# Kernel optimization log

Measured on AMD Instinct MI355X. Metric: run time of the kernel, lower is better.

## Reference

```python
import jax, jax.numpy as jnp
import numpy as np

N_HEADS = 8
D_K = 64
SCALE = D_K ** -0.5


def setup_inputs() -> dict:
    key = jax.random.key(0)
    ks = jax.random.split(key, 5)
    B, C, H, W = 4, 512, 32, 32
    x = jax.random.normal(ks[0], (B, C, H, W), dtype=jnp.float32)
    Wp = jax.random.normal(ks[1], (3 * N_HEADS * D_K, C), dtype=jnp.float32) * (C ** -0.5)
    bp = jax.random.normal(ks[2], (3 * N_HEADS * D_K,), dtype=jnp.float32) * 0.02
    Wo = jax.random.normal(ks[3], (C, N_HEADS * D_K), dtype=jnp.float32) * ((N_HEADS * D_K) ** -0.5)
    bo = jax.random.normal(ks[4], (C,), dtype=jnp.float32) * 0.02
    return {"x": x, "Wp": Wp, "bp": bp, "Wo": Wo, "bo": bo}


def reference(x, Wp, bp, Wo, bo):
    # x: [B, C, H, W]; NOTE: the torch module defines GroupNorm but never calls it.
    B, C, H, W = x.shape
    s = H * W
    xs = x.reshape(B, C, s).transpose(0, 2, 1)          # [B, s, C]
    qkv = (xs @ Wp.T + bp).reshape(B, s, N_HEADS, 3 * D_K)
    q, k, v = jnp.split(qkv, 3, axis=-1)                 # each [B, s, h, d]
    attn = jnp.einsum('bihd,bjhd->bijh', q, k) * SCALE   # [B, s, s, h]
    attn = jax.nn.softmax(attn, axis=2)                  # softmax over j (keys)
    res = jnp.einsum('bijh,bjhd->bihd', attn, v)         # [B, s, h, d]
    res = res.reshape(B, s, N_HEADS * D_K)
    out = res @ Wo.T + bo + xs                           # residual add
    return out.transpose(0, 2, 1).reshape(B, C, H, W)
```

## Files before the change

### kernel.cpp

```cpp
#include <hip/hip_runtime.h>
#include <hip/hip_bf16.h>

typedef unsigned short u16;
typedef __attribute__((ext_vector_type(8))) short frag_ab;
typedef __attribute__((ext_vector_type(4))) float f32x4;
typedef _Float16 f16;
typedef __attribute__((ext_vector_type(4))) _Float16 f16x4;

#define LOG2E 1.44269504088896f

__device__ __forceinline__ float fast_exp2(float x) {
    return __builtin_amdgcn_exp2f(x);
}

__device__ __forceinline__ void gload_lds16(const u16* g, u16* s) {
    __builtin_amdgcn_global_load_lds((const __attribute__((address_space(1))) void*)g,
                                     (__attribute__((address_space(3))) void*)s, 16, 0, 0);
}
__device__ __forceinline__ void gload_lds16h(const f16* g, f16* s) {
    __builtin_amdgcn_global_load_lds((const __attribute__((address_space(1))) void*)g,
                                     (__attribute__((address_space(3))) void*)s, 16, 0, 0);
}

__device__ __forceinline__ void gemm64x128_bt_mainloop(
    const u16* __restrict__ A, const u16* __restrict__ B, int K,
    int m0, int n0, f32x4 acc[2][4], u16* As, u16* Bs)
{
    const int tid = threadIdx.x;
    const int lane = tid & 63, quad = lane >> 4, l16 = lane & 15;
    const int wr = ((tid >> 7) & 1) * 32;
    const int wc = ((tid >> 6) & 1) * 64;
    const int srow = tid >> 3;
    const int scol = (tid & 7) * 8;

    for (int k0 = 0; k0 < K; k0 += 64) {
        __syncthreads();
        #pragma unroll
        for (int p = 0; p < 2; ++p) {
            const int r = srow + p * 32;
            gload_lds16(A + (size_t)(m0 + r) * K + k0 + scol, As + r * 64 + scol);
        }
        #pragma unroll
        for (int p = 0; p < 4; ++p) {
            const int r = srow + p * 32;
            gload_lds16(B + (size_t)(n0 + r) * K + k0 + scol, Bs + r * 64 + scol);
        }
        __syncthreads();
        #pragma unroll
        for (int ks = 0; ks < 2; ++ks) {
            frag_ab a[2], b[4];
            #pragma unroll
            for (int mt = 0; mt < 2; ++mt)
                a[mt] = *(const frag_ab*)(As + (wr + mt * 16 + l16) * 64 + ks * 32 + quad * 8);
            #pragma unroll
            for (int nt = 0; nt < 4; ++nt)
                b[nt] = *(const frag_ab*)(Bs + (wc + nt * 16 + l16) * 64 + ks * 32 + quad * 8);
            #pragma unroll
            for (int mt = 0; mt < 2; ++mt)
                #pragma unroll
                for (int nt = 0; nt < 4; ++nt)
                    acc[mt][nt] = __builtin_amdgcn_mfma_f32_16x16x32_bf16(a[mt], b[nt], acc[mt][nt], 0, 0, 0);
        }
    }
}

__device__ __forceinline__ void gemm64x64_bt_mainloop(
    const u16* __restrict__ A, const u16* __restrict__ B, int K,
    int m0, int n0, f32x4 acc[2][2], u16* As, u16* Bs)
{
    const int tid = threadIdx.x;
    const int lane = tid & 63, quad = lane >> 4, l16 = lane & 15;
    const int wr = ((tid >> 7) & 1) * 32;
    const int wc = ((tid >> 6) & 1) * 32;
    const int srow = tid >> 3;
    const int scol = (tid & 7) * 8;

    for (int k0 = 0; k0 < K; k0 += 64) {
        __syncthreads();
        #pragma unroll
        for (int p = 0; p < 2; ++p) {
            const int r = srow + p * 32;
            gload_lds16(A + (size_t)(m0 + r) * K + k0 + scol, As + r * 64 + scol);
            gload_lds16(B + (size_t)(n0 + r) * K + k0 + scol, Bs + r * 64 + scol);
        }
        __syncthreads();
        #pragma unroll
        for (int ks = 0; ks < 2; ++ks) {
            frag_ab a[2], b[2];
            #pragma unroll
            for (int mt = 0; mt < 2; ++mt)
                a[mt] = *(const frag_ab*)(As + (wr + mt * 16 + l16) * 64 + ks * 32 + quad * 8);
            #pragma unroll
            for (int nt = 0; nt < 2; ++nt)
                b[nt] = *(const frag_ab*)(Bs + (wc + nt * 16 + l16) * 64 + ks * 32 + quad * 8);
            #pragma unroll
            for (int mt = 0; mt < 2; ++mt)
                #pragma unroll
                for (int nt = 0; nt < 2; ++nt)
                    acc[mt][nt] = __builtin_amdgcn_mfma_f32_16x16x32_bf16(a[mt], b[nt], acc[mt][nt], 0, 0, 0);
        }
    }
}

__global__ __launch_bounds__(256) void prep_kernel(
    const float* __restrict__ x, __hip_bfloat16* __restrict__ xs_bf,
    const float* __restrict__ Wp, const float* __restrict__ Wo,
    __hip_bfloat16* __restrict__ w_bf)
{
    __shared__ float tile[32][33];
    const int tid = threadIdx.x;
    const int id = blockIdx.x;
    if (id < 2048) {
        const int i0 = (id & 31) * 32;
        const int c0 = ((id >> 5) & 15) * 32;
        const int b  = id >> 9;
        const int tx = tid & 31, ty = tid >> 5;
        const float* xp = x + ((size_t)b * 512 + c0) * 1024 + i0;
        #pragma unroll
        for (int r = ty; r < 32; r += 8)
            tile[r][tx] = xp[(size_t)r * 1024 + tx];
        __syncthreads();
        __hip_bfloat16* op = xs_bf + ((size_t)b * 1024 + i0) * 512 + c0;
        #pragma unroll
        for (int r = ty; r < 32; r += 8)
            op[(size_t)r * 512 + tx] = __float2bfloat16(tile[tx][r]);
    } else {
        const int t = (id - 2048) * 256 + tid;
        const int i4 = t * 4;
        const float* src = (i4 < 786432) ? (Wp + i4) : (Wo + (i4 - 786432));
        const float4 v = *(const float4*)src;
        ushort4 o;
        o.x = __bfloat16_as_ushort(__float2bfloat16(v.x));
        o.y = __bfloat16_as_ushort(__float2bfloat16(v.y));
        o.z = __bfloat16_as_ushort(__float2bfloat16(v.z));
        o.w = __bfloat16_as_ushort(__float2bfloat16(v.w));
        *(ushort4*)((u16*)w_bf + i4) = o;
    }
}

__global__ __launch_bounds__(256) void qkv_gemm_kernel(
    const u16* __restrict__ Wpb, const u16* __restrict__ xsb,
    const float* __restrict__ bp,
    u16* __restrict__ Qb, u16* __restrict__ Kb, f16* __restrict__ VtT)
{
    __shared__ u16 lds[12288];
    u16* As = lds;
    u16* Bs = lds + 4096;
    f32x4 acc[2][4];
    #pragma unroll
    for (int mt = 0; mt < 2; ++mt)
        #pragma unroll
        for (int nt = 0; nt < 4; ++nt)
            { acc[mt][nt][0]=0.f; acc[mt][nt][1]=0.f; acc[mt][nt][2]=0.f; acc[mt][nt][3]=0.f; }
    const int m0 = blockIdx.x * 64;
    const int n0 = blockIdx.y * 128;
    gemm64x128_bt_mainloop(Wpb, xsb, 512, m0, n0, acc, As, Bs);

    const int tid = threadIdx.x;
    const int lane = tid & 63, quad = lane >> 4, l16 = lane & 15;
    const int wr = ((tid >> 7) & 1) * 32, wc = ((tid >> 6) & 1) * 64;
    const int h = blockIdx.x / 3, part = blockIdx.x % 3;
    const int b = blockIdx.y >> 3, ipb = (blockIdx.y & 7) * 128;
    const size_t bh = (size_t)(b * 8 + h);

    if (part < 2) {
        const float scale = (part == 0) ? (0.125f * LOG2E) : 1.0f;
        __syncthreads();
        u16* T = lds;
        #pragma unroll
        for (int nt = 0; nt < 4; ++nt) {
            const int px = wc + nt * 16 + l16;
            #pragma unroll
            for (int mt = 0; mt < 2; ++mt) {
                const int cb = m0 + wr + mt * 16 + quad * 4;
                ushort4 pk;
                pk.x = __bfloat16_as_ushort(__float2bfloat16((acc[mt][nt][0] + bp[cb + 0]) * scale));
                pk.y = __bfloat16_as_ushort(__float2bfloat16((acc[mt][nt][1] + bp[cb + 1]) * scale));
                pk.z = __bfloat16_as_ushort(__float2bfloat16((acc[mt][nt][2] + bp[cb + 2]) * scale));
                pk.w = __bfloat16_as_ushort(__float2bfloat16((acc[mt][nt][3] + bp[cb + 3]) * scale));
                *(ushort4*)&T[px * 72 + wr + mt * 16 + quad * 4] = pk;
            }
        }
        __syncthreads();
        u16* dst = (part == 0 ? Qb : Kb);
        #pragma unroll
        for (int p = 0; p < 4; ++p) {
            const int row = p * 32 + (tid >> 3);
            const int ch8 = (tid & 7) * 8;
            uint4 rv = *(uint4*)&T[row * 72 + ch8];
            *(uint4*)(dst + ((bh * 1024 + ipb + row) << 6) + ch8) = rv;
        }
    } else {
        f16* dst = VtT + bh * 65536;
        #pragma unroll
        for (int mt = 0; mt < 2; ++mt) {
            #pragma unroll
            for (int r = 0; r < 4; ++r) {
                const int d = wr + mt * 16 + quad * 4 + r;
                const float bias = bp[m0 + d];
                #pragma unroll
                for (int nt = 0; nt < 4; ++nt) {
                    const int j = ipb + wc + nt * 16 + l16;
                    dst[(size_t)(j >> 3) * 512 + d * 8 + (j & 7)] =
                        (f16)(acc[mt][nt][r] + bias);
                }
            }
        }
    }
}

__global__ __launch_bounds__(256) void attn_kernel(
    const u16* __restrict__ Qb, const u16* __restrict__ Kb,
    const f16* __restrict__ VtT, __hip_bfloat16* __restrict__ resb)
{
    __shared__ u16 Ks[128 * 64];
    __shared__ f16 Vs[16 * 64 * 8];
    __shared__ float Opart[4][32][68];
    __shared__ float Lpart[4][4][16];
    const int bh = blockIdx.x;
    const int it = blockIdx.y;
    const int tid = threadIdx.x;
    const int w = tid >> 6, lane = tid & 63, quad = lane >> 4, l16 = lane & 15;
    const int srow = tid >> 3, scol = (tid & 7) * 8;

    const u16* Qp = Qb + (size_t)bh * 65536;
    const u16* Kp = Kb + (size_t)bh * 65536;
    const f16* Vp = VtT + (size_t)bh * 65536;

    frag_ab bq[4][2];
    #pragma unroll
    for (int ig = 0; ig < 4; ++ig) {
        const u16* qptr = Qp + (size_t)(it * 64 + ig * 16 + l16) * 64 + quad * 8;
        bq[ig][0] = *(const frag_ab*)(qptr);
        bq[ig][1] = *(const frag_ab*)(qptr + 32);
    }

    f32x4 o[4][4];
    #pragma unroll
    for (int ig = 0; ig < 4; ++ig)
        #pragma unroll
        for (int dt = 0; dt < 4; ++dt)
            { o[ig][dt][0]=0.f; o[ig][dt][1]=0.f; o[ig][dt][2]=0.f; o[ig][dt][3]=0.f; }
    float l_acc[4] = {0.f, 0.f, 0.f, 0.f};

    for (int jt = 0; jt < 8; ++jt) {
        __syncthreads();
        #pragma unroll
        for (int p = 0; p < 4; ++p) {
            const int r = srow + p * 32;
            gload_lds16(Kp + (size_t)(jt * 128 + r) * 64 + scol, Ks + r * 64 + scol);
        }
        #pragma unroll
        for (int p = 0; p < 4; ++p) {
            const int c = w * 4 + p;
            gload_lds16h(Vp + (size_t)((jt * 16 + c) * 64 + lane) * 8,
                         Vs + (size_t)(c * 64 + lane) * 8);
        }
        __syncthreads();

        frag_ab ka[2][2];
        #pragma unroll
        for (int mt = 0; mt < 2; ++mt) {
            const u16* kp = Ks + (w * 32 + mt * 16 + l16) * 64 + quad * 8;
            ka[mt][0] = *(const frag_ab*)(kp);
            ka[mt][1] = *(const frag_ab*)(kp + 32);
        }
        f16x4 va[4][2];
        #pragma unroll
        for (int ks = 0; ks < 2; ++ks) {
            const f16* vrow = Vs + (size_t)(w * 4 + ks * 2 + (quad >> 1)) * 512 + (quad & 1) * 4;
            #pragma unroll
            for (int dt = 0; dt < 4; ++dt)
                va[dt][ks] = *(const f16x4*)(vrow + (dt * 16 + l16) * 8);
        }
        #pragma unroll
        for (int ig = 0; ig < 4; ++ig) {
            f32x4 st0 = {0.f, 0.f, 0.f, 0.f}, st1 = {0.f, 0.f, 0.f, 0.f};
            st0 = __builtin_amdgcn_mfma_f32_16x16x32_bf16(ka[0][0], bq[ig][0], st0, 0, 0, 0);
            st0 = __builtin_amdgcn_mfma_f32_16x16x32_bf16(ka[0][1], bq[ig][1], st0, 0, 0, 0);
            st1 = __builtin_amdgcn_mfma_f32_16x16x32_bf16(ka[1][0], bq[ig][0], st1, 0, 0, 0);
            st1 = __builtin_amdgcn_mfma_f32_16x16x32_bf16(ka[1][1], bq[ig][1], st1, 0, 0, 0);
            f16x4 p0, p1;
            float s = 0.f;
            #pragma unroll
            for (int r = 0; r < 4; ++r) {
                const float e0 = fast_exp2(st0[r]);
                const float e1 = fast_exp2(st1[r]);
                s += e0 + e1;
                p0[r] = (f16)e0;
                p1[r] = (f16)e1;
            }
            l_acc[ig] += s;
            #pragma unroll
            for (int dt = 0; dt < 4; ++dt) {
                o[ig][dt] = __builtin_amdgcn_mfma_f32_16x16x16f16(va[dt][0], p0, o[ig][dt], 0, 0, 0);
                o[ig][dt] = __builtin_amdgcn_mfma_f32_16x16x16f16(va[dt][1], p1, o[ig][dt], 0, 0, 0);
            }
        }
    }
    #pragma unroll
    for (int ig = 0; ig < 4; ++ig) {
        l_acc[ig] += __shfl_xor(l_acc[ig], 16);
        l_acc[ig] += __shfl_xor(l_acc[ig], 32);
    }
    if (lane < 16) {
        #pragma unroll
        for (int ig = 0; ig < 4; ++ig)
            Lpart[w][ig][lane] = l_acc[ig];
    }

    const int bb = bh >> 3, hh = bh & 7;
    const int il = tid >> 3, d0 = (tid & 7) * 8;
    #pragma unroll
    for (int ph = 0; ph < 2; ++ph) {
        __syncthreads();
        #pragma unroll
        for (int g = 0; g < 2; ++g) {
            const int ig = ph * 2 + g;
            #pragma unroll
            for (int dt = 0; dt < 4; ++dt)
                *(f32x4*)&Opart[w][g * 16 + l16][dt * 16 + quad * 4] = o[ig][dt];
        }
        __syncthreads();
        f32x4 sa = *(const f32x4*)&Opart[0][il][d0];
        f32x4 sb = *(const f32x4*)&Opart[0][il][d0 + 4];
        #pragma unroll
        for (int ww = 1; ww < 4; ++ww) {
            sa += *(const f32x4*)&Opart[ww][il][d0];
            sb += *(const f32x4*)&Opart[ww][il][d0 + 4];
        }
        const int ig = ph * 2 + (il >> 4);
        const float linv = 1.f / (Lpart[0][ig][il & 15] + Lpart[1][ig][il & 15] +
                                  Lpart[2][ig][il & 15] + Lpart[3][ig][il & 15]);
        u16 pk[8];
        #pragma unroll
        for (int e = 0; e < 4; ++e) {
            pk[e]     = __bfloat16_as_ushort(__float2bfloat16(sa[e] * linv));
            pk[e + 4] = __bfloat16_as_ushort(__float2bfloat16(sb[e] * linv));
        }
        u16* orow = (u16*)resb +
            ((size_t)(bb * 1024 + it * 64 + ph * 32 + il)) * 512 + hh * 64 + d0;
        *(uint4*)orow = *(uint4*)pk;
    }
}

__global__ __launch_bounds__(256) void out_gemm_kernel(
    const u16* __restrict__ Wob, const u16* __restrict__ resb,
    const float* __restrict__ bo, const float* __restrict__ x,
    float* __restrict__ out)
{
    __shared__ u16 As[64 * 64];
    __shared__ u16 Bs[64 * 64];
    f32x4 acc[2][2];
    #pragma unroll
    for (int mt = 0; mt < 2; ++mt)
        #pragma unroll
        for (int nt = 0; nt < 2; ++nt)
            { acc[mt][nt][0]=0.f; acc[mt][nt][1]=0.f; acc[mt][nt][2]=0.f; acc[mt][nt][3]=0.f; }
    const int m0 = blockIdx.x * 64;
    const int n0 = blockIdx.y * 64;
    gemm64x64_bt_mainloop(Wob, resb, 512, m0, n0, acc, As, Bs);

    const int tid = threadIdx.x;
    const int lane = tid & 63, quad = lane >> 4, l16 = lane & 15;
    const int wr = ((tid >> 7) & 1) * 32, wc = ((tid >> 6) & 1) * 32;
    #pragma unroll
    for (int nt = 0; nt < 2; ++nt) {
        const int pix = n0 + wc + nt * 16 + l16;
        const int b = pix >> 10, ip = pix & 1023;
        #pragma unroll
        for (int mt = 0; mt < 2; ++mt) {
            #pragma unroll
            for (int r = 0; r < 4; ++r) {
                const int c = m0 + wr + mt * 16 + quad * 4 + r;
                const size_t oidx = (((size_t)b * 512 + c) << 10) + ip;
                out[oidx] = acc[mt][nt][r] + bo[c] + x[oidx];
            }
        }
    }
}

extern "C" void kernel_launch(void* const* d_in, const int* in_sizes, int n_in,
                              void* d_out, int out_size, void* d_ws, size_t ws_size,
                              hipStream_t stream)
{
    const float* x  = (const float*)d_in[0];
    const float* Wp = (const float*)d_in[1];
    const float* bp = (const float*)d_in[2];
    const float* Wo = (const float*)d_in[3];
    const float* bo = (const float*)d_in[4];
    float* out = (float*)d_out;

    char* ws = (char*)d_ws;
    size_t off = 0;
    auto carve = [&](size_t bytes) -> void* {
        void* ptr = ws + off;
        off += (bytes + 255) & ~(size_t)255;
        return ptr;
    };
    __hip_bfloat16* xs_bf = (__hip_bfloat16*)carve((size_t)4096 * 512 * 2);
    __hip_bfloat16* Wp_bf = (__hip_bfloat16*)carve((size_t)1536 * 512 * 2);
    __hip_bfloat16* Wo_bf = (__hip_bfloat16*)carve((size_t)512 * 512 * 2);
    u16*            Qb    = (u16*)carve((size_t)32 * 1024 * 64 * 2);
    u16*            Kb    = (u16*)carve((size_t)32 * 1024 * 64 * 2);
    f16*            VtT   = (f16*)carve((size_t)32 * 1024 * 64 * 2);
    __hip_bfloat16* resb  = (__hip_bfloat16*)carve((size_t)4096 * 512 * 2);

    prep_kernel<<<dim3(3072), 256, 0, stream>>>(x, xs_bf, Wp, Wo, Wp_bf);
    qkv_gemm_kernel<<<dim3(24, 32), 256, 0, stream>>>(
        (const u16*)Wp_bf, (const u16*)xs_bf, bp, Qb, Kb, VtT);
    attn_kernel<<<dim3(32, 16), 256, 0, stream>>>(Qb, Kb, VtT, resb);
    out_gemm_kernel<<<dim3(8, 64), 256, 0, stream>>>(
        (const u16*)Wo_bf, (const u16*)resb, bo, x, out);
    (void)Wo_bf; (void)ws_size; (void)in_sizes; (void)n_in; (void)out_size;
}
```

Before: 114.5 us.

## Widen GEMM K-tiles to 128 and shrink attention LDS footprint

The shared GEMM mainloop helpers are inlined into the QKV and output projection kernels, and the K step grows from 64 to 128. This halves the number of barrier-separated load/compute iterations, at the cost of twice the LDS per block. The attention kernel now reuses its K/V LDS buffer for the output-partial reduction instead of a separate Opart array, which cuts LDS use and may allow more blocks per CU. The epilogue is reorganised into four 16-row phases with narrower stores, which adds more barriers.

```diff
diff --git a/kernel.cpp b/kernel.cpp
--- a/kernel.cpp
+++ b/kernel.cpp
@@ -20,86 +20,6 @@
 __device__ __forceinline__ void gload_lds16h(const f16* g, f16* s) {
     __builtin_amdgcn_global_load_lds((const __attribute__((address_space(1))) void*)g,
                                      (__attribute__((address_space(3))) void*)s, 16, 0, 0);
-}
-
-__device__ __forceinline__ void gemm64x128_bt_mainloop(
-    const u16* __restrict__ A, const u16* __restrict__ B, int K,
-    int m0, int n0, f32x4 acc[2][4], u16* As, u16* Bs)
-{
-    const int tid = threadIdx.x;
-    const int lane = tid & 63, quad = lane >> 4, l16 = lane & 15;
-    const int wr = ((tid >> 7) & 1) * 32;
-    const int wc = ((tid >> 6) & 1) * 64;
-    const int srow = tid >> 3;
-    const int scol = (tid & 7) * 8;
-
-    for (int k0 = 0; k0 < K; k0 += 64) {
-        __syncthreads();
-        #pragma unroll
-        for (int p = 0; p < 2; ++p) {
-            const int r = srow + p * 32;
-            gload_lds16(A + (size_t)(m0 + r) * K + k0 + scol, As + r * 64 + scol);
-        }
-        #pragma unroll
-        for (int p = 0; p < 4; ++p) {
-            const int r = srow + p * 32;
-            gload_lds16(B + (size_t)(n0 + r) * K + k0 + scol, Bs + r * 64 + scol);
-        }
-        __syncthreads();
-        #pragma unroll
-        for (int ks = 0; ks < 2; ++ks) {
-            frag_ab a[2], b[4];
-            #pragma unroll
-            for (int mt = 0; mt < 2; ++mt)
-                a[mt] = *(const frag_ab*)(As + (wr + mt * 16 + l16) * 64 + ks * 32 + quad * 8);
-            #pragma unroll
-            for (int nt = 0; nt < 4; ++nt)
-                b[nt] = *(const frag_ab*)(Bs + (wc + nt * 16 + l16) * 64 + ks * 32 + quad * 8);
-            #pragma unroll
-            for (int mt = 0; mt < 2; ++mt)
-                #pragma unroll
-                for (int nt = 0; nt < 4; ++nt)
-                    acc[mt][nt] = __builtin_amdgcn_mfma_f32_16x16x32_bf16(a[mt], b[nt], acc[mt][nt], 0, 0, 0);
-        }
-    }
-}
-
-__device__ __forceinline__ void gemm64x64_bt_mainloop(
-    const u16* __restrict__ A, const u16* __restrict__ B, int K,
-    int m0, int n0, f32x4 acc[2][2], u16* As, u16* Bs)
-{
-    const int tid = threadIdx.x;
-    const int lane = tid & 63, quad = lane >> 4, l16 = lane & 15;
-    const int wr = ((tid >> 7) & 1) * 32;
-    const int wc = ((tid >> 6) & 1) * 32;
-    const int srow = tid >> 3;
-    const int scol = (tid & 7) * 8;
-
-    for (int k0 = 0; k0 < K; k0 += 64) {
-        __syncthreads();
-        #pragma unroll
-        for (int p = 0; p < 2; ++p) {
-            const int r = srow + p * 32;
-            gload_lds16(A + (size_t)(m0 + r) * K + k0 + scol, As + r * 64 + scol);
-            gload_lds16(B + (size_t)(n0 + r) * K + k0 + scol, Bs + r * 64 + scol);
-        }
-        __syncthreads();
-        #pragma unroll
-        for (int ks = 0; ks < 2; ++ks) {
-            frag_ab a[2], b[2];
-            #pragma unroll
-            for (int mt = 0; mt < 2; ++mt)
-                a[mt] = *(const frag_ab*)(As + (wr + mt * 16 + l16) * 64 + ks * 32 + quad * 8);
-            #pragma unroll
-            for (int nt = 0; nt < 2; ++nt)
-                b[nt] = *(const frag_ab*)(Bs + (wc + nt * 16 + l16) * 64 + ks * 32 + quad * 8);
-            #pragma unroll
-            for (int mt = 0; mt < 2; ++mt)
-                #pragma unroll
-                for (int nt = 0; nt < 2; ++nt)
-                    acc[mt][nt] = __builtin_amdgcn_mfma_f32_16x16x32_bf16(a[mt], b[nt], acc[mt][nt], 0, 0, 0);
-        }
-    }
 }
 
 __global__ __launch_bounds__(256) void prep_kernel(
@@ -143,9 +63,9 @@
     const float* __restrict__ bp,
     u16* __restrict__ Qb, u16* __restrict__ Kb, f16* __restrict__ VtT)
 {
-    __shared__ u16 lds[12288];
+    __shared__ u16 lds[24576];
     u16* As = lds;
-    u16* Bs = lds + 4096;
+    u16* Bs = lds + 8192;
     f32x4 acc[2][4];
     #pragma unroll
     for (int mt = 0; mt < 2; ++mt)
@@ -154,11 +74,43 @@
             { acc[mt][nt][0]=0.f; acc[mt][nt][1]=0.f; acc[mt][nt][2]=0.f; acc[mt][nt][3]=0.f; }
     const int m0 = blockIdx.x * 64;
     const int n0 = blockIdx.y * 128;
-    gemm64x128_bt_mainloop(Wpb, xsb, 512, m0, n0, acc, As, Bs);
 
     const int tid = threadIdx.x;
     const int lane = tid & 63, quad = lane >> 4, l16 = lane & 15;
     const int wr = ((tid >> 7) & 1) * 32, wc = ((tid >> 6) & 1) * 64;
+    const int srow = tid >> 4;
+    const int scol = (tid & 15) * 8;
+
+    for (int k0 = 0; k0 < 512; k0 += 128) {
+        __syncthreads();
+        #pragma unroll
+        for (int p = 0; p < 4; ++p) {
+            const int r = srow + p * 16;
+            gload_lds16(Wpb + (size_t)(m0 + r) * 512 + k0 + scol, As + r * 128 + scol);
+        }
+        #pragma unroll
+        for (int p = 0; p < 8; ++p) {
+            const int r = srow + p * 16;
+            gload_lds16(xsb + (size_t)(n0 + r) * 512 + k0 + scol, Bs + r * 128 + scol);
+        }
+        __syncthreads();
+        #pragma unroll
+        for (int ks = 0; ks < 4; ++ks) {
+            frag_ab a[2], b[4];
+            #pragma unroll
+            for (int mt = 0; mt < 2; ++mt)
+                a[mt] = *(const frag_ab*)(As + (wr + mt * 16 + l16) * 128 + ks * 32 + quad * 8);
+            #pragma unroll
+            for (int nt = 0; nt < 4; ++nt)
+                b[nt] = *(const frag_ab*)(Bs + (wc + nt * 16 + l16) * 128 + ks * 32 + quad * 8);
+            #pragma unroll
+            for (int mt = 0; mt < 2; ++mt)
+                #pragma unroll
+                for (int nt = 0; nt < 4; ++nt)
+                    acc[mt][nt] = __builtin_amdgcn_mfma_f32_16x16x32_bf16(a[mt], b[nt], acc[mt][nt], 0, 0, 0);
+        }
+    }
+
     const int h = blockIdx.x / 3, part = blockIdx.x % 3;
     const int b = blockIdx.y >> 3, ipb = (blockIdx.y & 7) * 128;
     const size_t bh = (size_t)(b * 8 + h);
@@ -213,10 +165,10 @@
     const u16* __restrict__ Qb, const u16* __restrict__ Kb,
     const f16* __restrict__ VtT, __hip_bfloat16* __restrict__ resb)
 {
-    __shared__ u16 Ks[128 * 64];
-    __shared__ f16 Vs[16 * 64 * 8];
-    __shared__ float Opart[4][32][68];
+    __shared__ u16 pool[16384];
     __shared__ float Lpart[4][4][16];
+    u16* Ks = pool;
+    f16* Vs = (f16*)(pool + 8192);
     const int bh = blockIdx.x;
     const int it = blockIdx.y;
     const int tid = threadIdx.x;
@@ -309,38 +261,29 @@
             Lpart[w][ig][lane] = l_acc[ig];
     }
 
+    float* Op = (float*)pool;
     const int bb = bh >> 3, hh = bh & 7;
-    const int il = tid >> 3, d0 = (tid & 7) * 8;
-    #pragma unroll
-    for (int ph = 0; ph < 2; ++ph) {
-        __syncthreads();
-        #pragma unroll
-        for (int g = 0; g < 2; ++g) {
-            const int ig = ph * 2 + g;
-            #pragma unroll
-            for (int dt = 0; dt < 4; ++dt)
-                *(f32x4*)&Opart[w][g * 16 + l16][dt * 16 + quad * 4] = o[ig][dt];
-        }
-        __syncthreads();
-        f32x4 sa = *(const f32x4*)&Opart[0][il][d0];
-        f32x4 sb = *(const f32x4*)&Opart[0][il][d0 + 4];
-        #pragma unroll
-        for (int ww = 1; ww < 4; ++ww) {
-            sa += *(const f32x4*)&Opart[ww][il][d0];
-            sb += *(const f32x4*)&Opart[ww][il][d0 + 4];
-        }
-        const int ig = ph * 2 + (il >> 4);
-        const float linv = 1.f / (Lpart[0][ig][il & 15] + Lpart[1][ig][il & 15] +
-                                  Lpart[2][ig][il & 15] + Lpart[3][ig][il & 15]);
-        u16 pk[8];
-        #pragma unroll
-        for (int e = 0; e < 4; ++e) {
-            pk[e]     = __bfloat16_as_ushort(__float2bfloat16(sa[e] * linv));
-            pk[e + 4] = __bfloat16_as_ushort(__float2bfloat16(sb[e] * linv));
-        }
+    const int ri = tid >> 4, d0f = (tid & 15) * 4;
+    #pragma unroll
+    for (int ph = 0; ph < 4; ++ph) {
+        __syncthreads();
+        #pragma unroll
+        for (int dt = 0; dt < 4; ++dt)
+            *(f32x4*)&Op[(w * 16 + l16) * 68 + dt * 16 + quad * 4] = o[ph][dt];
+        __syncthreads();
+        f32x4 s = *(const f32x4*)&Op[ri * 68 + d0f];
+        #pragma unroll
+        for (int ww = 1; ww < 4; ++ww)
+            s += *(const f32x4*)&Op[(ww * 16 + ri) * 68 + d0f];
+        const float linv = 1.f / (Lpart[0][ph][ri] + Lpart[1][ph][ri] +
+                                  Lpart[2][ph][ri] + Lpart[3][ph][ri]);
+        u16 pk[4];
+        #pragma unroll
+        for (int e = 0; e < 4; ++e)
+            pk[e] = __bfloat16_as_ushort(__float2bfloat16(s[e] * linv));
         u16* orow = (u16*)resb +
-            ((size_t)(bb * 1024 + it * 64 + ph * 32 + il)) * 512 + hh * 64 + d0;
-        *(uint4*)orow = *(uint4*)pk;
+            ((size_t)(bb * 1024 + it * 64 + ph * 16 + ri)) * 512 + hh * 64 + d0f;
+        *(uint2*)orow = *(uint2*)pk;
     }
 }
 
@@ -349,8 +292,8 @@
     const float* __restrict__ bo, const float* __restrict__ x,
     float* __restrict__ out)
 {
-    __shared__ u16 As[64 * 64];
-    __shared__ u16 Bs[64 * 64];
+    __shared__ u16 As[64 * 128];
+    __shared__ u16 Bs[64 * 128];
     f32x4 acc[2][2];
     #pragma unroll
     for (int mt = 0; mt < 2; ++mt)
@@ -359,11 +302,39 @@
             { acc[mt][nt][0]=0.f; acc[mt][nt][1]=0.f; acc[mt][nt][2]=0.f; acc[mt][nt][3]=0.f; }
     const int m0 = blockIdx.x * 64;
     const int n0 = blockIdx.y * 64;
-    gemm64x64_bt_mainloop(Wob, resb, 512, m0, n0, acc, As, Bs);
 
     const int tid = threadIdx.x;
     const int lane = tid & 63, quad = lane >> 4, l16 = lane & 15;
     const int wr = ((tid >> 7) & 1) * 32, wc = ((tid >> 6) & 1) * 32;
+    const int srow = tid >> 4;
+    const int scol = (tid & 15) * 8;
+
+    for (int k0 = 0; k0 < 512; k0 += 128) {
+        __syncthreads();
+        #pragma unroll
+        for (int p = 0; p < 4; ++p) {
+            const int r = srow + p * 16;
+            gload_lds16(Wob + (size_t)(m0 + r) * 512 + k0 + scol, As + r * 128 + scol);
+            gload_lds16(resb + (size_t)(n0 + r) * 512 + k0 + scol, Bs + r * 128 + scol);
+        }
+        __syncthreads();
+        #pragma unroll
+        for (int ks = 0; ks < 4; ++ks) {
+            frag_ab a[2], b[2];
+            #pragma unroll
+            for (int mt = 0; mt < 2; ++mt)
+                a[mt] = *(const frag_ab*)(As + (wr + mt * 16 + l16) * 128 + ks * 32 + quad * 8);
+            #pragma unroll
+            for (int nt = 0; nt < 2; ++nt)
+                b[nt] = *(const frag_ab*)(Bs + (wc + nt * 16 + l16) * 128 + ks * 32 + quad * 8);
+            #pragma unroll
+            for (int mt = 0; mt < 2; ++mt)
+                #pragma unroll
+                for (int nt = 0; nt < 2; ++nt)
+                    acc[mt][nt] = __builtin_amdgcn_mfma_f32_16x16x32_bf16(a[mt], b[nt], acc[mt][nt], 0, 0, 0);
+        }
+    }
+
     #pragma unroll
     for (int nt = 0; nt < 2; ++nt) {
         const int pix = n0 + wc + nt * 16 + l16;
```

Result: slower. 121.4 us (+6.0%).

## Halve attention query tile and alias output-reduction buffer onto K/V LDS

Applied to the files above, without the earlier changes.

Each attention block now handles 32 queries instead of 64, which doubles the grid to 1024 blocks and halves the per-thread accumulator registers. The cross-wave output reduction buffer now reuses the K/V shared-memory pool instead of having its own allocation, cutting LDS per block from about 66KB to 32KB. Both changes aim to raise occupancy and parallelism across the CUs. The cost is that K/V tiles are loaded from global memory twice as often relative to the query work, so each block does less MFMA work per byte loaded.

```diff
diff --git a/kernel.cpp b/kernel.cpp
--- a/kernel.cpp
+++ b/kernel.cpp
@@ -213,10 +213,10 @@
     const u16* __restrict__ Qb, const u16* __restrict__ Kb,
     const f16* __restrict__ VtT, __hip_bfloat16* __restrict__ resb)
 {
-    __shared__ u16 Ks[128 * 64];
-    __shared__ f16 Vs[16 * 64 * 8];
-    __shared__ float Opart[4][32][68];
-    __shared__ float Lpart[4][4][16];
+    __shared__ u16 pool[16384];
+    __shared__ float Lpart[4][2][16];
+    u16* Ks = pool;
+    f16* Vs = (f16*)(pool + 8192);
     const int bh = blockIdx.x;
     const int it = blockIdx.y;
     const int tid = threadIdx.x;
@@ -227,21 +227,21 @@
     const u16* Kp = Kb + (size_t)bh * 65536;
     const f16* Vp = VtT + (size_t)bh * 65536;
 
-    frag_ab bq[4][2];
-    #pragma unroll
-    for (int ig = 0; ig < 4; ++ig) {
-        const u16* qptr = Qp + (size_t)(it * 64 + ig * 16 + l16) * 64 + quad * 8;
+    frag_ab bq[2][2];
+    #pragma unroll
+    for (int ig = 0; ig < 2; ++ig) {
+        const u16* qptr = Qp + (size_t)(it * 32 + ig * 16 + l16) * 64 + quad * 8;
         bq[ig][0] = *(const frag_ab*)(qptr);
         bq[ig][1] = *(const frag_ab*)(qptr + 32);
     }
 
-    f32x4 o[4][4];
-    #pragma unroll
-    for (int ig = 0; ig < 4; ++ig)
+    f32x4 o[2][4];
+    #pragma unroll
+    for (int ig = 0; ig < 2; ++ig)
         #pragma unroll
         for (int dt = 0; dt < 4; ++dt)
             { o[ig][dt][0]=0.f; o[ig][dt][1]=0.f; o[ig][dt][2]=0.f; o[ig][dt][3]=0.f; }
-    float l_acc[4] = {0.f, 0.f, 0.f, 0.f};
+    float l_acc[2] = {0.f, 0.f};
 
     for (int jt = 0; jt < 8; ++jt) {
         __syncthreads();
@@ -274,7 +274,7 @@
                 va[dt][ks] = *(const f16x4*)(vrow + (dt * 16 + l16) * 8);
         }
         #pragma unroll
-        for (int ig = 0; ig < 4; ++ig) {
+        for (int ig = 0; ig < 2; ++ig) {
             f32x4 st0 = {0.f, 0.f, 0.f, 0.f}, st1 = {0.f, 0.f, 0.f, 0.f};
             st0 = __builtin_amdgcn_mfma_f32_16x16x32_bf16(ka[0][0], bq[ig][0], st0, 0, 0, 0);
             st0 = __builtin_amdgcn_mfma_f32_16x16x32_bf16(ka[0][1], bq[ig][1], st0, 0, 0, 0);
@@ -299,48 +299,39 @@
         }
     }
     #pragma unroll
-    for (int ig = 0; ig < 4; ++ig) {
+    for (int ig = 0; ig < 2; ++ig) {
         l_acc[ig] += __shfl_xor(l_acc[ig], 16);
         l_acc[ig] += __shfl_xor(l_acc[ig], 32);
     }
     if (lane < 16) {
         #pragma unroll
-        for (int ig = 0; ig < 4; ++ig)
+        for (int ig = 0; ig < 2; ++ig)
             Lpart[w][ig][lane] = l_acc[ig];
     }
 
+    float* Op = (float*)pool;
     const int bb = bh >> 3, hh = bh & 7;
-    const int il = tid >> 3, d0 = (tid & 7) * 8;
+    const int ri = tid >> 4, d0f = (tid & 15) * 4;
     #pragma unroll
     for (int ph = 0; ph < 2; ++ph) {
         __syncthreads();
         #pragma unroll
-        for (int g = 0; g < 2; ++g) {
-            const int ig = ph * 2 + g;
-            #pragma unroll
-            for (int dt = 0; dt < 4; ++dt)
-                *(f32x4*)&Opart[w][g * 16 + l16][dt * 16 + quad * 4] = o[ig][dt];
-        }
-        __syncthreads();
-        f32x4 sa = *(const f32x4*)&Opart[0][il][d0];
-        f32x4 sb = *(const f32x4*)&Opart[0][il][d0 + 4];
-        #pragma unroll
-        for (int ww = 1; ww < 4; ++ww) {
-            sa += *(const f32x4*)&Opart[ww][il][d0];
-            sb += *(const f32x4*)&Opart[ww][il][d0 + 4];
-        }
-        const int ig = ph * 2 + (il >> 4);
-        const float linv = 1.f / (Lpart[0][ig][il & 15] + Lpart[1][ig][il & 15] +
-                                  Lpart[2][ig][il & 15] + Lpart[3][ig][il & 15]);
-        u16 pk[8];
-        #pragma unroll
-        for (int e = 0; e < 4; ++e) {
-            pk[e]     = __bfloat16_as_ushort(__float2bfloat16(sa[e] * linv));
-            pk[e + 4] = __bfloat16_as_ushort(__float2bfloat16(sb[e] * linv));
-        }
+        for (int dt = 0; dt < 4; ++dt)
+            *(f32x4*)&Op[(w * 16 + l16) * 68 + dt * 16 + quad * 4] = o[ph][dt];
+        __syncthreads();
+        f32x4 s = *(const f32x4*)&Op[ri * 68 + d0f];
+        #pragma unroll
+        for (int ww = 1; ww < 4; ++ww)
+            s += *(const f32x4*)&Op[(ww * 16 + ri) * 68 + d0f];
+        const float linv = 1.f / (Lpart[0][ph][ri] + Lpart[1][ph][ri] +
+                                  Lpart[2][ph][ri] + Lpart[3][ph][ri]);
+        u16 pk[4];
+        #pragma unroll
+        for (int e = 0; e < 4; ++e)
+            pk[e] = __bfloat16_as_ushort(__float2bfloat16(s[e] * linv));
         u16* orow = (u16*)resb +
-            ((size_t)(bb * 1024 + it * 64 + ph * 32 + il)) * 512 + hh * 64 + d0;
-        *(uint4*)orow = *(uint4*)pk;
+            ((size_t)(bb * 1024 + it * 32 + ph * 16 + ri)) * 512 + hh * 64 + d0f;
+        *(uint2*)orow = *(uint2*)pk;
     }
 }
 
@@ -409,7 +400,7 @@
     prep_kernel<<<dim3(3072), 256, 0, stream>>>(x, xs_bf, Wp, Wo, Wp_bf);
     qkv_gemm_kernel<<<dim3(24, 32), 256, 0, stream>>>(
         (const u16*)Wp_bf, (const u16*)xs_bf, bp, Qb, Kb, VtT);
-    attn_kernel<<<dim3(32, 16), 256, 0, stream>>>(Qb, Kb, VtT, resb);
+    attn_kernel<<<dim3(32, 32), 256, 0, stream>>>(Qb, Kb, VtT, resb);
     out_gemm_kernel<<<dim3(8, 64), 256, 0, stream>>>(
         (const u16*)Wo_bf, (const u16*)resb, bo, x, out);
     (void)Wo_bf; (void)ws_size; (void)in_sizes; (void)n_in; (void)out_size;
```

New measurement: 118.6 us. 3.5% more time.
